# Kernel tuning notes

Hardware: AMD Instinct MI355X
Metric: run time of the kernel (lower is better)

The kernel has to match this reference:

```python
import jax, jax.numpy as jnp
import numpy as np
import math

N, E, O, C, KD, KEYD = 50000, 800000, 4, 64, 16, 128


def setup_inputs() -> dict:
    key = jax.random.key(0)
    ks = jax.random.split(key, 10)
    x = jax.random.normal(ks[0], (N, O, C), jnp.float32)
    kernel_basis = jax.random.normal(ks[1], (E, O, KD), jnp.float32)
    fiber_kernel_basis = jax.random.normal(ks[2], (O, O, KD), jnp.float32)
    edge_index = jax.random.randint(ks[3], (2, E), 0, N, jnp.int32)
    # nn.Linear default init ~ U(-1/sqrt(fan_in), 1/sqrt(fan_in)); scaled normal is fine as data
    kernel_W = jax.random.normal(ks[4], (C, KD), jnp.float32) / math.sqrt(KD)        # kernel: Linear(kernel_dim -> in_channels)
    fiber_kernel_W = jax.random.normal(ks[5], (C, KD), jnp.float32) / math.sqrt(KD)  # depthwise: in*out/groups = C
    key_W = jax.random.normal(ks[6], (KEYD, C), jnp.float32) / math.sqrt(C)
    key_b = jnp.zeros((KEYD,), jnp.float32)
    query_W = jax.random.normal(ks[7], (KEYD, C), jnp.float32) / math.sqrt(C)
    query_b = jnp.zeros((KEYD,), jnp.float32)
    bias = jnp.zeros((C,), jnp.float32)
    return {"x": x, "kernel_basis": kernel_basis, "fiber_kernel_basis": fiber_kernel_basis,
            "edge_index": edge_index, "kernel_W": kernel_W, "fiber_kernel_W": fiber_kernel_W,
            "key_W": key_W, "key_b": key_b, "query_W": query_W, "query_b": query_b, "bias": bias}


def reference(x, kernel_basis, fiber_kernel_basis, edge_index, kernel_W, fiber_kernel_W,
              key_W, key_b, query_W, query_b, bias):
    src = edge_index[0]
    dst = edge_index[1]
    n = x.shape[0]
    # per-edge spatial kernel: [E,O,KD] @ [KD,C] -> [E,O,C]
    k = jnp.einsum('eok,ck->eoc', kernel_basis, kernel_W)
    message = x[src] * k                                       # [E,O,C]
    # scatter-softmax attention over incoming edges of each target node
    keys = jnp.einsum('noc,kc->nok', x, key_W) + key_b        # [N,O,KEYD]
    queries = jnp.einsum('noc,kc->nok', x, query_W) + query_b
    logits = jnp.sum(keys[src] * queries[dst], axis=-1, keepdims=True) / math.sqrt(KEYD)  # [E,O,1]
    e = jnp.exp(logits - jnp.max(logits))                      # global-max stabilization, as in source
    denom = jax.ops.segment_sum(e, dst, num_segments=n) + 1e-6 # [N,O,1]
    att = e / denom[dst]
    message = message * att
    # scatter-add aggregation into target nodes
    x1 = jax.ops.segment_sum(message, dst, num_segments=n)     # [N,O,C]
    # fiber (orientation) mixing kernel: [O,O,KD] @ [KD,C] -> [O,O,C]
    fk = jnp.einsum('pok,ck->poc', fiber_kernel_basis, fiber_kernel_W)
    x2 = jnp.einsum('boc,poc->bpc', x1, fk) / fk.shape[-2]
    return x2 + bias
```

## Files before the change

kernel.cpp:

```cpp
#include <hip/hip_runtime.h>
#include <math.h>

#define NN 50000
#define EE 800000
#define OO 4
#define CC 64
#define KDD 16
#define KEYDD 128
#define CH 16

typedef float v2f __attribute__((ext_vector_type(2)));

__device__ __forceinline__ float wave_red_sum(float v) {
  int x;
  x = __builtin_amdgcn_update_dpp(0, __float_as_int(v), 0x111, 0xf, 0xf, false);
  v += __int_as_float(x);
  x = __builtin_amdgcn_update_dpp(0, __float_as_int(v), 0x112, 0xf, 0xf, false);
  v += __int_as_float(x);
  x = __builtin_amdgcn_update_dpp(0, __float_as_int(v), 0x114, 0xf, 0xf, false);
  v += __int_as_float(x);
  x = __builtin_amdgcn_update_dpp(0, __float_as_int(v), 0x118, 0xf, 0xf, false);
  v += __int_as_float(x);
  x = __builtin_amdgcn_update_dpp(0, __float_as_int(v), 0x142, 0xa, 0xf, false);
  v += __int_as_float(x);
  x = __builtin_amdgcn_update_dpp(0, __float_as_int(v), 0x143, 0xc, 0xf, false);
  v += __int_as_float(x);
  return __int_as_float(__builtin_amdgcn_readlane(__float_as_int(v), 63));
}

__device__ __forceinline__ float exp2_fast(float x) {
  float r;
  asm("v_exp_f32 %0, %1" : "=v"(r) : "v"(x));
  return r;
}

__device__ __forceinline__ void red4(float q0, float q1, float q2, float q3,
                                     float& p0, float& p1, float& p2, float& p3) {
  asm("s_nop 1\n\tv_permlane32_swap_b32 %0, %1" : "+v"(q0), "+v"(q1));
  float ra = q0 + q1;
  asm("s_nop 1\n\tv_permlane32_swap_b32 %0, %1" : "+v"(q2), "+v"(q3));
  float rb = q2 + q3;
  asm("s_nop 1\n\t"
      "v_add_f32_dpp %0, %0, %0 row_shr:1 row_mask:0xf bank_mask:0xf bound_ctrl:0\n\t"
      "v_add_f32_dpp %1, %1, %1 row_shr:1 row_mask:0xf bank_mask:0xf bound_ctrl:0\n\t"
      "v_add_f32_dpp %0, %0, %0 row_shr:2 row_mask:0xf bank_mask:0xf bound_ctrl:0\n\t"
      "v_add_f32_dpp %1, %1, %1 row_shr:2 row_mask:0xf bank_mask:0xf bound_ctrl:0\n\t"
      "v_add_f32_dpp %0, %0, %0 row_shr:4 row_mask:0xf bank_mask:0xf bound_ctrl:0\n\t"
      "v_add_f32_dpp %1, %1, %1 row_shr:4 row_mask:0xf bank_mask:0xf bound_ctrl:0\n\t"
      "v_add_f32_dpp %0, %0, %0 row_shr:8 row_mask:0xf bank_mask:0xf bound_ctrl:0\n\t"
      "v_add_f32_dpp %1, %1, %1 row_shr:8 row_mask:0xf bank_mask:0xf bound_ctrl:0\n\t"
      "v_add_f32_dpp %0, %0, %0 row_bcast:15 row_mask:0xa bank_mask:0xf bound_ctrl:0\n\t"
      "v_add_f32_dpp %1, %1, %1 row_bcast:15 row_mask:0xa bank_mask:0xf bound_ctrl:0\n\t"
      "s_nop 0"
      : "+v"(ra), "+v"(rb));
  p0 = __int_as_float(__builtin_amdgcn_readlane(__float_as_int(ra), 31));
  p1 = __int_as_float(__builtin_amdgcn_readlane(__float_as_int(ra), 63));
  p2 = __int_as_float(__builtin_amdgcn_readlane(__float_as_int(rb), 31));
  p3 = __int_as_float(__builtin_amdgcn_readlane(__float_as_int(rb), 63));
}

__global__ void prep_kernel(const float* __restrict__ keyW, const float* __restrict__ keyB,
                            const float* __restrict__ qryW, const float* __restrict__ qryB,
                            const float* __restrict__ fkb, const float* __restrict__ fkw,
                            float* __restrict__ Mt, float* __restrict__ aVec,
                            float* __restrict__ bVec, float* __restrict__ c0,
                            float* __restrict__ fk) {
  __shared__ float qw[KEYDD * CC];
  __shared__ float kws[KEYDD * 4];
  int t = threadIdx.x, b = blockIdx.x;
  if (b < 16) {
    for (int i = t; i < KEYDD * CC; i += 256) qw[i] = qryW[i];
    for (int i = t; i < KEYDD * 4; i += 256) {
      int k = i >> 2, c1l = i & 3;
      kws[i] = keyW[k * CC + b * 4 + c1l];
    }
    __syncthreads();
    int c1l = t >> 6, c2 = t & 63;
    float s = 0.f;
    #pragma unroll 8
    for (int k = 0; k < KEYDD; ++k)
      s = fmaf(kws[k * 4 + c1l], qw[k * CC + c2], s);
    Mt[c2 * CC + b * 4 + c1l] = s;
  } else {
    if (t < CC) {
      float sa = 0.f, sb = 0.f;
      for (int k = 0; k < KEYDD; ++k) {
        sa = fmaf(keyB[k], qryW[k * CC + t], sa);
        sb = fmaf(qryB[k], keyW[k * CC + t], sb);
      }
      aVec[t] = sa; bVec[t] = sb;
    }
    if (t == 0) {
      float s = 0.f;
      for (int k = 0; k < KEYDD; ++k) s = fmaf(keyB[k], qryB[k], s);
      c0[0] = s;
    }
    for (int idx = t; idx < OO * OO * CC; idx += 256) {
      int p = idx >> 8, rem = idx & 255;
      int o = rem >> 6, c = rem & 63;
      float s = 0.f;
      #pragma unroll
      for (int kd = 0; kd < KDD; ++kd)
        s = fmaf(fkb[(p * OO + o) * KDD + kd], fkw[c * KDD + kd], s);
      fk[idx] = 0.25f * s;
    }
  }
}

__global__ void count_kernel(const int* __restrict__ ei, int* __restrict__ counts) {
  int e = blockIdx.x * 256 + threadIdx.x;
  if (e < EE) atomicAdd(&counts[ei[EE + e]], 1);
}

__global__ void scan1_kernel(const int* __restrict__ counts, int* __restrict__ incl,
                             int* __restrict__ bsum, int n) {
  __shared__ int buf[256];
  int t = threadIdx.x;
  int i = blockIdx.x * 256 + t;
  int v = (i < n) ? counts[i] : 0;
  buf[t] = v;
  __syncthreads();
  for (int off = 1; off < 256; off <<= 1) {
    int a = buf[t];
    int b2 = (t >= off) ? buf[t - off] : 0;
    __syncthreads();
    buf[t] = a + b2;
    __syncthreads();
  }
  if (i < n) incl[i] = buf[t];
  if (t == 255) bsum[blockIdx.x] = buf[255];
}
__global__ void scan2_kernel(const int* __restrict__ bsum, int* __restrict__ bbase, int nb) {
  __shared__ int buf[256];
  int t = threadIdx.x;
  int v = (t < nb) ? bsum[t] : 0;
  buf[t] = v;
  __syncthreads();
  for (int off = 1; off < 256; off <<= 1) {
    int a = buf[t];
    int b2 = (t >= off) ? buf[t - off] : 0;
    __syncthreads();
    buf[t] = a + b2;
    __syncthreads();
  }
  if (t < nb) bbase[t] = buf[t] - v;
}
__global__ void scan3_kernel(const int* __restrict__ counts, const int* __restrict__ incl,
                             const int* __restrict__ bbase, int* __restrict__ offsets, int n) {
  int i = blockIdx.x * 256 + threadIdx.x;
  if (i < n) {
    int oi = bbase[blockIdx.x] + incl[i];
    offsets[i] = oi - counts[i];
    if (i == n - 1) offsets[n] = oi;
  }
}

__global__ void fill_kernel(const int* __restrict__ ei, const int* __restrict__ offsets,
                            int* __restrict__ counts, long long* __restrict__ pairs) {
  int e = blockIdx.x * 256 + threadIdx.x;
  if (e < EE) {
    int d = ei[EE + e];
    int r = atomicSub(&counts[d], 1) - 1;
    int pos = offsets[d] + r;
    pairs[pos] = ((long long)ei[e] << 32) | (unsigned)e;
  }
}

__device__ __forceinline__ float kv_dot(const float* __restrict__ kb, int ej, int obase,
                                        float4 kw0, float4 kw1, float4 kw2, float4 kw3) {
  const float4* bp = reinterpret_cast<const float4*>(kb + ej * (OO * KDD) + obase);
  float4 b0 = bp[0], b1 = bp[1], b2 = bp[2], b3 = bp[3];
  v2f a0 = {0.f, 0.f}, a1 = {0.f, 0.f};
  #define P2(f4, i) (reinterpret_cast<const v2f*>(&(f4))[i])
  a0 = __builtin_elementwise_fma(P2(b0, 0), P2(kw0, 0), a0);
  a1 = __builtin_elementwise_fma(P2(b0, 1), P2(kw0, 1), a1);
  a0 = __builtin_elementwise_fma(P2(b1, 0), P2(kw1, 0), a0);
  a1 = __builtin_elementwise_fma(P2(b1, 1), P2(kw1, 1), a1);
  a0 = __builtin_elementwise_fma(P2(b2, 0), P2(kw2, 0), a0);
  a1 = __builtin_elementwise_fma(P2(b2, 1), P2(kw2, 1), a1);
  a0 = __builtin_elementwise_fma(P2(b3, 0), P2(kw3, 0), a0);
  a1 = __builtin_elementwise_fma(P2(b3, 1), P2(kw3, 1), a1);
  #undef P2
  v2f s = a0 + a1;
  return s.x + s.y;
}

__global__ __launch_bounds__(256, 4) void mega_kernel(
    const float* __restrict__ x, const float* __restrict__ Mt,
    const float* __restrict__ aVec, const float* __restrict__ bVec,
    const float* __restrict__ c0p, const float* __restrict__ kb,
    const float* __restrict__ kW, const int* __restrict__ offsets,
    const long long* __restrict__ pairs, const float* __restrict__ fkg,
    const float* __restrict__ bias, float* __restrict__ out) {
  __shared__ float xs[OO * CC];
  __shared__ float x1[OO * CC];
  int n = blockIdx.x;
  int t = threadIdx.x;
  int o = __builtin_amdgcn_readfirstlane(t >> 6);
  int c = t & 63;
  const float scale2 = 0.12751541050862828f;
  int js = offsets[n], je = offsets[n + 1];
  int deg = je - js;

  float xown = x[(size_t)n * (OO * CC) + t];
  xs[t] = xown;
  __syncthreads();

  int lane16 = c & 15;
  long long pr = 0;
  if (deg > 0) pr = pairs[js + min(lane16, deg - 1)];

  float ubr = 0.f;
  #pragma unroll 8
  for (int c2 = 0; c2 < CC; ++c2)
    ubr = fmaf(Mt[c2 * CC + c], xs[o * CC + c2], ubr);
  ubr += bVec[c];
  float base2 = (wave_red_sum(aVec[c] * xown) + c0p[0]) * scale2;

  const float4* kwp = reinterpret_cast<const float4*>(kW + c * KDD);
  float4 kw0 = kwp[0], kw1 = kwp[1], kw2 = kwp[2], kw3 = kwp[3];
  int obase = o * KDD;
  int voff = c << 2;

  float m2 = -INFINITY, S = 0.f, acc = 0.f;

  for (int cs = 0; cs < deg; cs += CH) {
    int cl = deg - cs; if (cl > CH) cl = CH;
    int e_v = (int)((unsigned long long)pr & 0xffffffffu);
    int s_v = (int)(pr >> 32);
    float xv[CH];
    #pragma unroll
    for (int j = 0; j < CH; ++j) {
      int sj = __builtin_amdgcn_readlane(s_v, j);
      const float* pj = x + (size_t)(sj * OO + o) * CC;
      asm volatile("global_load_dword %0, %1, %2"
                   : "=v"(xv[j]) : "v"(voff), "s"(pj));
    }
    asm volatile("s_waitcnt vmcnt(0)" ::: "memory");
    __builtin_amdgcn_sched_barrier(0);
    int ns = cs + CH;
    if (ns < deg) {
      int ncl = deg - ns;
      pr = pairs[js + ns + min(lane16, ncl - 1)];
    }
    __builtin_amdgcn_sched_barrier(0);
    #define SUB4(J0)                                                           \
    {                                                                          \
      float kv0 = kv_dot(kb, __builtin_amdgcn_readlane(e_v, (J0) + 0), obase, kw0, kw1, kw2, kw3); \
      float kv1 = kv_dot(kb, __builtin_amdgcn_readlane(e_v, (J0) + 1), obase, kw0, kw1, kw2, kw3); \
      float kv2 = kv_dot(kb, __builtin_amdgcn_readlane(e_v, (J0) + 2), obase, kw0, kw1, kw2, kw3); \
      float kv3 = kv_dot(kb, __builtin_amdgcn_readlane(e_v, (J0) + 3), obase, kw0, kw1, kw2, kw3); \
      float p0, p1, p2, p3;                                                    \
      red4(xv[(J0) + 0] * ubr, xv[(J0) + 1] * ubr,                             \
           xv[(J0) + 2] * ubr, xv[(J0) + 3] * ubr, p0, p1, p2, p3);            \
      float l0 = ((J0) + 0 < cl) ? fmaf(p0, scale2, base2) : -INFINITY;        \
      float l1 = ((J0) + 1 < cl) ? fmaf(p1, scale2, base2) : -INFINITY;        \
      float l2 = ((J0) + 2 < cl) ? fmaf(p2, scale2, base2) : -INFINITY;        \
      float l3 = ((J0) + 3 < cl) ? fmaf(p3, scale2, base2) : -INFINITY;        \
      float cm = fmaxf(fmaxf(l0, l1), fmaxf(l2, l3));                          \
      if (cm > m2) {                                                           \
        float rsc = exp2_fast(m2 - cm);                                        \
        S *= rsc; acc *= rsc; m2 = cm;                                         \
      }                                                                        \
      float ev0 = exp2_fast(l0 - m2);                                          \
      float ev1 = exp2_fast(l1 - m2);                                          \
      float ev2 = exp2_fast(l2 - m2);                                          \
      float ev3 = exp2_fast(l3 - m2);                                          \
      S += (ev0 + ev1) + (ev2 + ev3);                                          \
      acc = fmaf(ev0 * kv0, xv[(J0) + 0], acc);                                \
      acc = fmaf(ev1 * kv1, xv[(J0) + 1], acc);                                \
      acc = fmaf(ev2 * kv2, xv[(J0) + 2], acc);                                \
      acc = fmaf(ev3 * kv3, xv[(J0) + 3], acc);                                \
    }
    SUB4(0)
    if (cl > 4)  SUB4(4)
    if (cl > 8)  SUB4(8)
    if (cl > 12) SUB4(12)
    #undef SUB4
  }

  float invd = 1.0f / (S + 1e-6f);
  x1[t] = acc * invd;
  __syncthreads();
  float s2s = 0.f;
  #pragma unroll
  for (int oo = 0; oo < OO; ++oo)
    s2s = fmaf(x1[oo * CC + c], fkg[o * (OO * CC) + oo * CC + c], s2s);
  out[(size_t)n * (OO * CC) + t] = s2s + bias[c];
}

extern "C" void kernel_launch(void* const* d_in, const int* in_sizes, int n_in,
                              void* d_out, int out_size, void* d_ws, size_t ws_size,
                              hipStream_t stream) {
  const float* x    = (const float*)d_in[0];
  const float* kb   = (const float*)d_in[1];
  const float* fkb  = (const float*)d_in[2];
  const int*   ei   = (const int*)d_in[3];
  const float* kW   = (const float*)d_in[4];
  const float* fkW  = (const float*)d_in[5];
  const float* keyW = (const float*)d_in[6];
  const float* keyB = (const float*)d_in[7];
  const float* qryW = (const float*)d_in[8];
  const float* qryB = (const float*)d_in[9];
  const float* bias = (const float*)d_in[10];
  float* out = (float*)d_out;

  const int NB = (NN + 255) / 256;

  float* wsf  = (float*)d_ws;
  float* Mt   = wsf;
  float* aVec = Mt + 4096;
  float* bVec = aVec + 64;
  float* c0   = bVec + 64;
  float* fk   = c0 + 64;
  long long* pairs = (long long*)(fk + 1024);
  int* counts    = (int*)(pairs + EE);
  int* offsets   = counts + NN;
  int* incl      = offsets + NN + 1;
  int* bsum      = incl + NN;
  int* bbase     = bsum + 256;

  hipMemsetAsync(counts, 0, (size_t)NN * sizeof(int), stream);

  prep_kernel<<<17, 256, 0, stream>>>(keyW, keyB, qryW, qryB, fkb, fkW, Mt, aVec, bVec, c0, fk);
  count_kernel<<<(EE + 255) / 256, 256, 0, stream>>>(ei, counts);
  scan1_kernel<<<NB, 256, 0, stream>>>(counts, incl, bsum, NN);
  scan2_kernel<<<1, 256, 0, stream>>>(bsum, bbase, NB);
  scan3_kernel<<<NB, 256, 0, stream>>>(counts, incl, bbase, offsets, NN);
  fill_kernel<<<(EE + 255) / 256, 256, 0, stream>>>(ei, offsets, counts, pairs);
  mega_kernel<<<NN, 256, 0, stream>>>(x, Mt, aVec, bVec, c0, kb, kW, offsets, pairs,
                                      fk, bias, out);
}
```

Measured before the change: 422.0 us.

## Drop online-softmax max tracking and compute query projection from global loads

Removes the running-max rescaling in the per-node softmax: logits are exponentiated directly after factoring out the per-node base term, and the epsilon in the denominator is rescaled by exp2(-base2) to compensate. It also removes the shared-memory staging and the first block barrier for the node's own features, computing the projected query vector with four independent accumulators that read the row through a uniform pointer. This cuts per-edge compare, branch and rescale work and the startup sync, but without max subtraction exp2 of the raw logits can overflow or underflow when logits are large.

Measured after the change: 407.5 us, median of 2. 1.04x faster.

```diff
diff --git a/kernel.cpp b/kernel.cpp
--- a/kernel.cpp
+++ b/kernel.cpp
@@ -192,7 +192,6 @@
     const float* __restrict__ kW, const int* __restrict__ offsets,
     const long long* __restrict__ pairs, const float* __restrict__ fkg,
     const float* __restrict__ bias, float* __restrict__ out) {
-  __shared__ float xs[OO * CC];
   __shared__ float x1[OO * CC];
   int n = blockIdx.x;
   int t = threadIdx.x;
@@ -202,19 +201,22 @@
   int js = offsets[n], je = offsets[n + 1];
   int deg = je - js;
 
-  float xown = x[(size_t)n * (OO * CC) + t];
-  xs[t] = xown;
-  __syncthreads();
-
   int lane16 = c & 15;
   long long pr = 0;
   if (deg > 0) pr = pairs[js + min(lane16, deg - 1)];
 
-  float ubr = 0.f;
-  #pragma unroll 8
-  for (int c2 = 0; c2 < CC; ++c2)
-    ubr = fmaf(Mt[c2 * CC + c], xs[o * CC + c2], ubr);
-  ubr += bVec[c];
+  int rowoff = __builtin_amdgcn_readfirstlane((n * OO + o) * CC);
+  const float* xrow = x + rowoff;
+  float ub0 = 0.f, ub1 = 0.f, ub2 = 0.f, ub3 = 0.f;
+  #pragma unroll
+  for (int q = 0; q < 16; ++q) {
+    ub0 = fmaf(Mt[(4 * q + 0) * CC + c], xrow[4 * q + 0], ub0);
+    ub1 = fmaf(Mt[(4 * q + 1) * CC + c], xrow[4 * q + 1], ub1);
+    ub2 = fmaf(Mt[(4 * q + 2) * CC + c], xrow[4 * q + 2], ub2);
+    ub3 = fmaf(Mt[(4 * q + 3) * CC + c], xrow[4 * q + 3], ub3);
+  }
+  float ubr = (((ub0 + ub1) + (ub2 + ub3)) + bVec[c]) * scale2;
+  float xown = xrow[c];
   float base2 = (wave_red_sum(aVec[c] * xown) + c0p[0]) * scale2;
 
   const float4* kwp = reinterpret_cast<const float4*>(kW + c * KDD);
@@ -222,7 +224,7 @@
   int obase = o * KDD;
   int voff = c << 2;
 
-  float m2 = -INFINITY, S = 0.f, acc = 0.f;
+  float S = 0.f, acc = 0.f;
 
   for (int cs = 0; cs < deg; cs += CH) {
     int cl = deg - cs; if (cl > CH) cl = CH;
@@ -253,19 +255,10 @@
       float p0, p1, p2, p3;                                                    \
       red4(xv[(J0) + 0] * ubr, xv[(J0) + 1] * ubr,                             \
            xv[(J0) + 2] * ubr, xv[(J0) + 3] * ubr, p0, p1, p2, p3);            \
-      float l0 = ((J0) + 0 < cl) ? fmaf(p0, scale2, base2) : -INFINITY;        \
-      float l1 = ((J0) + 1 < cl) ? fmaf(p1, scale2, base2) : -INFINITY;        \
-      float l2 = ((J0) + 2 < cl) ? fmaf(p2, scale2, base2) : -INFINITY;        \
-      float l3 = ((J0) + 3 < cl) ? fmaf(p3, scale2, base2) : -INFINITY;        \
-      float cm = fmaxf(fmaxf(l0, l1), fmaxf(l2, l3));                          \
-      if (cm > m2) {                                                           \
-        float rsc = exp2_fast(m2 - cm);                                        \
-        S *= rsc; acc *= rsc; m2 = cm;                                         \
-      }                                                                        \
-      float ev0 = exp2_fast(l0 - m2);                                          \
-      float ev1 = exp2_fast(l1 - m2);                                          \
-      float ev2 = exp2_fast(l2 - m2);                                          \
-      float ev3 = exp2_fast(l3 - m2);                                          \
+      float ev0 = ((J0) + 0 < cl) ? exp2_fast(p0) : 0.f;                       \
+      float ev1 = ((J0) + 1 < cl) ? exp2_fast(p1) : 0.f;                       \
+      float ev2 = ((J0) + 2 < cl) ? exp2_fast(p2) : 0.f;                       \
+      float ev3 = ((J0) + 3 < cl) ? exp2_fast(p3) : 0.f;                       \
       S += (ev0 + ev1) + (ev2 + ev3);                                          \
       acc = fmaf(ev0 * kv0, xv[(J0) + 0], acc);                                \
       acc = fmaf(ev1 * kv1, xv[(J0) + 1], acc);                                \
@@ -279,7 +272,7 @@
     #undef SUB4
   }
 
-  float invd = 1.0f / (S + 1e-6f);
+  float invd = 1.0f / (S + 1e-6f * exp2_fast(-base2));
   x1[t] = acc * invd;
   __syncthreads();
   float s2s = 0.f;
```
